# Kernel tuning notes

Hardware: AMD Instinct MI355X
Metric: run time of the kernel (lower is better)

Reference implementation:

```python
import jax, jax.numpy as jnp
import numpy as np

B, D, H, G = 32768, 768, 256, 8
GS = D // G          # group size = 96
MIN_G, MAX_G = 2, 6  # min/max active groups


def setup_inputs() -> dict:
    key = jax.random.key(0)
    ks = jax.random.split(key, 12)
    s = 0.02
    return {
        "query_embedding": jax.random.normal(ks[0], (B, D), jnp.float32),
        # router_net: Linear(D,H) -> LayerNorm(H) -> GELU -> Linear(H,H//2) -> GELU -> Linear(H//2,G)
        "w1": jax.random.normal(ks[1], (D, H), jnp.float32) * s,
        "b1": jnp.zeros((H,), jnp.float32),
        "ln_g": jnp.ones((H,), jnp.float32),
        "ln_b": jnp.zeros((H,), jnp.float32),
        "w2": jax.random.normal(ks[2], (H, H // 2), jnp.float32) * s,
        "b2": jnp.zeros((H // 2,), jnp.float32),
        "w3": jax.random.normal(ks[3], (H // 2, G), jnp.float32) * s,
        "b3": jnp.zeros((G,), jnp.float32),
        # dim_importance: Linear(D,H) -> GELU -> Linear(H,D) (bias init 2.0) -> Sigmoid
        "dw1": jax.random.normal(ks[4], (D, H), jnp.float32) * s,
        "db1": jnp.zeros((H,), jnp.float32),
        "dw2": jax.random.normal(ks[5], (H, D), jnp.float32) * s,
        "db2": jnp.full((D,), 2.0, jnp.float32),
        "group_importance": jax.random.normal(ks[6], (G,), jnp.float32) * s,
    }


def _gelu(x):
    return jax.nn.gelu(x, approximate=False)  # torch nn.GELU default = exact erf


def _layernorm(x, g, b, eps=1e-5):
    mu = jnp.mean(x, axis=-1, keepdims=True)
    var = jnp.var(x, axis=-1, keepdims=True)
    return (x - mu) * jax.lax.rsqrt(var + eps) * g + b


def reference(query_embedding, w1, b1, ln_g, ln_b, w2, b2, w3, b3,
              dw1, db1, dw2, db2, group_importance):
    x = query_embedding
    # router_net (eval mode: dropout is identity, sigmoid gating not gumbel)
    h1 = _gelu(_layernorm(x @ w1 + b1, ln_g, ln_b))
    h2 = _gelu(h1 @ w2 + b2)
    group_logits = h2 @ w3 + b3 + group_importance          # [B, G]
    group_probs = jax.nn.sigmoid(group_logits)

    # constrained hard selection: top MIN_G always on; ranks MIN_G..MAX_G-1 on iff prob > 0.5
    order = jnp.argsort(-group_probs, axis=-1)              # descending sort indices [B, G]
    sorted_probs = jnp.take_along_axis(group_probs, order, axis=-1)
    ranks = jnp.arange(G)
    act_sorted = jnp.where(ranks < MIN_G, 1.0,
                           jnp.where(ranks < MAX_G,
                                     (sorted_probs > 0.5).astype(jnp.float32), 0.0))
    b_idx = jnp.arange(x.shape[0])[:, None]
    hard_mask = jnp.zeros_like(group_probs).at[b_idx, order].set(act_sorted)
    # straight-through estimator
    group_selection = hard_mask - jax.lax.stop_gradient(group_probs) + group_probs

    # expand each group decision over its group_size dims -> [B, D]
    group_mask = jnp.repeat(group_selection, GS, axis=-1)

    dim_weights = jax.nn.sigmoid(_gelu(x @ dw1 + db1) @ dw2 + db2)  # [B, D]
    mask = group_mask * dim_weights

    active_groups = jnp.mean(jnp.sum((group_probs > 0.5).astype(jnp.float32), axis=-1))
    group_usage = jnp.mean((group_probs > 0.5).astype(jnp.float32), axis=0)
    f = jnp.mean(group_probs, axis=0)
    load_balance = G * jnp.sum(f * (1.0 / G))
    active_dims = jnp.mean(jnp.sum((mask > 0.5).astype(jnp.float32), axis=-1))

    return (mask, group_mask, dim_weights, group_probs, group_selection,
            active_groups, group_usage, load_balance, active_dims)
```

## Files before the change

kernel.cpp:

```cpp
#include <hip/hip_runtime.h>
#include <math.h>

#define NB 32768
#define ND 768
#define NH 256
#define NG 8
#define GSZ 96

typedef __attribute__((ext_vector_type(8))) short short8_t;
typedef __attribute__((ext_vector_type(4))) float f32x4;

__device__ __forceinline__ float gelu_exact(float v) {
    return 0.5f * v * (1.0f + erff(v * 0.7071067811865475f));
}
__device__ __forceinline__ float sigmoidf_(float v) {
    return 1.0f / (1.0f + expf(-v));
}
__device__ __forceinline__ unsigned short f2bf(float f) {
    union { float f; unsigned u; } a; a.f = f;
    unsigned r = a.u + 0x7FFF + ((a.u >> 16) & 1);
    return (unsigned short)(r >> 16);
}
__device__ __forceinline__ void f2bf2(float f, unsigned short& hi, unsigned short& lo) {
    union { float f; unsigned u; } a; a.f = f;
    unsigned r = a.u + 0x7FFF + ((a.u >> 16) & 1);
    hi = (unsigned short)(r >> 16);
    union { unsigned u; float f; } hf; hf.u = (r >> 16) << 16;
    float rem = f - hf.f;
    union { float f; unsigned u; } b; b.f = rem;
    unsigned r2 = b.u + 0x7FFF + ((b.u >> 16) & 1);
    lo = (unsigned short)(r2 >> 16);
}

__global__ __launch_bounds__(256) void cvt_wall(
    const float* __restrict__ w1, const float* __restrict__ dw1,
    const float* __restrict__ dw2, const float* __restrict__ w2,
    unsigned short* __restrict__ w1Th, unsigned short* __restrict__ w1Tl,
    unsigned short* __restrict__ dw1T, unsigned short* __restrict__ dw2T,
    unsigned short* __restrict__ w2Th, unsigned short* __restrict__ w2Tl,
    float* __restrict__ scal)
{
    const int b = blockIdx.x, t = threadIdx.x;
    if (b < 96) {
        int idx = b * 256 + t;
        int k8 = idx >> 8, c = idx & 255;
        short8_t h, lo;
        #pragma unroll
        for (int j = 0; j < 8; ++j) {
            unsigned short hi_, lo_;
            f2bf2(w1[(size_t)(k8 * 8 + j) * 256 + c], hi_, lo_);
            h[j] = (short)hi_; lo[j] = (short)lo_;
        }
        *(short8_t*)(w1Th + (size_t)c * 768 + k8 * 8) = h;
        *(short8_t*)(w1Tl + (size_t)c * 768 + k8 * 8) = lo;
    } else if (b < 192) {
        int idx = (b - 96) * 256 + t;
        int k8 = idx >> 8, c = idx & 255;
        short8_t h;
        #pragma unroll
        for (int j = 0; j < 8; ++j)
            h[j] = (short)f2bf(dw1[(size_t)(k8 * 8 + j) * 256 + c]);
        *(short8_t*)(dw1T + (size_t)c * 768 + k8 * 8) = h;
    } else if (b < 288) {
        int idx = (b - 192) * 256 + t;
        int k8 = idx / 768, c = idx - k8 * 768;
        short8_t h;
        #pragma unroll
        for (int j = 0; j < 8; ++j)
            h[j] = (short)f2bf(dw2[(size_t)(k8 * 8 + j) * 768 + c]);
        *(short8_t*)(dw2T + (size_t)c * 256 + k8 * 8) = h;
    } else if (b < 304) {
        int idx = (b - 288) * 256 + t;
        int k8 = idx >> 7, c = idx & 127;
        short8_t h, lo;
        #pragma unroll
        for (int j = 0; j < 8; ++j) {
            unsigned short hi_, lo_;
            f2bf2(w2[(size_t)(k8 * 8 + j) * 128 + c], hi_, lo_);
            h[j] = (short)hi_; lo[j] = (short)lo_;
        }
        *(short8_t*)(w2Th + (size_t)c * 256 + k8 * 8) = h;
        *(short8_t*)(w2Tl + (size_t)c * 256 + k8 * 8) = lo;
    } else {
        if (t < 11) scal[t] = 0.0f;
    }
}

__global__ __launch_bounds__(256) void mfma_u1(
    const float* __restrict__ x, const unsigned short* __restrict__ BTh,
    const unsigned short* __restrict__ BTl, float* __restrict__ u1)
{
    __shared__ unsigned short Ah[128][40];
    __shared__ unsigned short Al[128][40];
    __shared__ unsigned short Bh[128][40];
    __shared__ unsigned short Bl[128][40];

    const int tid = threadIdx.x;
    const int l = tid & 63;
    const int w = tid >> 6;
    const int wm = w >> 1, wn = w & 1;
    const int lg = l >> 4, lr = l & 15;
    const int rb = blockIdx.x >> 1;
    const int cb = blockIdx.x & 1;
    const int rowsBase = rb * 128, colBase = cb * 128;

    f32x4 acc[4][4];
    #pragma unroll
    for (int mi = 0; mi < 4; ++mi)
        #pragma unroll
        for (int ni = 0; ni < 4; ++ni) acc[mi][ni] = (f32x4){0.f, 0.f, 0.f, 0.f};

    for (int kb = 0; kb < ND; kb += 32) {
        #pragma unroll
        for (int m = 0; m < 2; ++m) {
            int flat = m * 256 + tid;
            int row = flat >> 2, seg = flat & 3;
            const float* src = x + (size_t)(rowsBase + row) * ND + kb + seg * 8;
            float4 v0 = *(const float4*)src;
            float4 v1 = *(const float4*)(src + 4);
            float f[8] = {v0.x, v0.y, v0.z, v0.w, v1.x, v1.y, v1.z, v1.w};
            short8_t ph, pl;
            #pragma unroll
            for (int j = 0; j < 8; ++j) {
                unsigned short hi_, lo_;
                f2bf2(f[j], hi_, lo_);
                ph[j] = (short)hi_; pl[j] = (short)lo_;
            }
            *(short8_t*)&Ah[row][seg * 8] = ph;
            *(short8_t*)&Al[row][seg * 8] = pl;
        }
        #pragma unroll
        for (int m = 0; m < 2; ++m) {
            int flat = m * 256 + tid;
            int col = flat >> 2, seg = flat & 3;
            size_t off = (size_t)(colBase + col) * ND + kb + seg * 8;
            *(short8_t*)&Bh[col][seg * 8] = *(const short8_t*)(BTh + off);
            *(short8_t*)&Bl[col][seg * 8] = *(const short8_t*)(BTl + off);
        }
        __syncthreads();

        short8_t afh[4], afl[4], bfh[4], bfl[4];
        #pragma unroll
        for (int mi = 0; mi < 4; ++mi) {
            afh[mi] = *(const short8_t*)&Ah[wm * 64 + mi * 16 + lr][lg * 8];
            afl[mi] = *(const short8_t*)&Al[wm * 64 + mi * 16 + lr][lg * 8];
        }
        #pragma unroll
        for (int ni = 0; ni < 4; ++ni) {
            bfh[ni] = *(const short8_t*)&Bh[wn * 64 + ni * 16 + lr][lg * 8];
            bfl[ni] = *(const short8_t*)&Bl[wn * 64 + ni * 16 + lr][lg * 8];
        }
        #pragma unroll
        for (int mi = 0; mi < 4; ++mi)
            #pragma unroll
            for (int ni = 0; ni < 4; ++ni) {
                acc[mi][ni] = __builtin_amdgcn_mfma_f32_16x16x32_bf16(
                    afl[mi], bfh[ni], acc[mi][ni], 0, 0, 0);
                acc[mi][ni] = __builtin_amdgcn_mfma_f32_16x16x32_bf16(
                    afh[mi], bfl[ni], acc[mi][ni], 0, 0, 0);
                acc[mi][ni] = __builtin_amdgcn_mfma_f32_16x16x32_bf16(
                    afh[mi], bfh[ni], acc[mi][ni], 0, 0, 0);
            }
        __syncthreads();
    }

    #pragma unroll
    for (int ni = 0; ni < 4; ++ni) {
        int col = colBase + wn * 64 + ni * 16 + lr;
        #pragma unroll
        for (int mi = 0; mi < 4; ++mi) {
            int rbase = rowsBase + wm * 64 + mi * 16 + lg * 4;
            #pragma unroll
            for (int j = 0; j < 4; ++j)
                u1[(size_t)(rbase + j) * 256 + col] = acc[mi][ni][j];
        }
    }
}

__global__ __launch_bounds__(256) void k1_epi(
    const float* __restrict__ u1, const float* __restrict__ b1,
    const float* __restrict__ lng, const float* __restrict__ lnb,
    float* __restrict__ h1)
{
    const int wv = threadIdx.x >> 6, l = threadIdx.x & 63;
    const int row = blockIdx.x * 4 + wv;
    float4 a = *(const float4*)(u1 + (size_t)row * 256 + l * 4);
    float4 bb = *(const float4*)(b1 + l * 4);
    float u[4] = {a.x + bb.x, a.y + bb.y, a.z + bb.z, a.w + bb.w};
    float s = u[0] + u[1] + u[2] + u[3];
    float q = u[0]*u[0] + u[1]*u[1] + u[2]*u[2] + u[3]*u[3];
    #pragma unroll
    for (int o = 1; o < 64; o <<= 1) {
        s += __shfl_xor(s, o);
        q += __shfl_xor(q, o);
    }
    float mean = s * (1.0f / 256.0f);
    float var  = q * (1.0f / 256.0f) - mean * mean;
    float rstd = rsqrtf(var + 1e-5f);
    float4 g = *(const float4*)(lng + l * 4);
    float4 be = *(const float4*)(lnb + l * 4);
    float4 o;
    o.x = gelu_exact((u[0] - mean) * rstd * g.x + be.x);
    o.y = gelu_exact((u[1] - mean) * rstd * g.y + be.y);
    o.z = gelu_exact((u[2] - mean) * rstd * g.z + be.z);
    o.w = gelu_exact((u[3] - mean) * rstd * g.w + be.w);
    *(float4*)(h1 + (size_t)row * 256 + l * 4) = o;
}

__global__ __launch_bounds__(256) void mfma_u2(
    const float* __restrict__ h1, const unsigned short* __restrict__ BTh,
    const unsigned short* __restrict__ BTl, float* __restrict__ u2)
{
    __shared__ unsigned short Ah[128][40];
    __shared__ unsigned short Al[128][40];
    __shared__ unsigned short Bh[128][40];
    __shared__ unsigned short Bl[128][40];

    const int tid = threadIdx.x;
    const int l = tid & 63;
    const int w = tid >> 6;
    const int wm = w >> 1, wn = w & 1;
    const int lg = l >> 4, lr = l & 15;
    const int rowsBase = blockIdx.x * 128;

    f32x4 acc[4][4];
    #pragma unroll
    for (int mi = 0; mi < 4; ++mi)
        #pragma unroll
        for (int ni = 0; ni < 4; ++ni) acc[mi][ni] = (f32x4){0.f, 0.f, 0.f, 0.f};

    for (int kb = 0; kb < 256; kb += 32) {
        #pragma unroll
        for (int m = 0; m < 2; ++m) {
            int flat = m * 256 + tid;
            int row = flat >> 2, seg = flat & 3;
            const float* src = h1 + (size_t)(rowsBase + row) * 256 + kb + seg * 8;
            float4 v0 = *(const float4*)src;
            float4 v1 = *(const float4*)(src + 4);
            float f[8] = {v0.x, v0.y, v0.z, v0.w, v1.x, v1.y, v1.z, v1.w};
            short8_t ph, pl;
            #pragma unroll
            for (int j = 0; j < 8; ++j) {
                unsigned short hi_, lo_;
                f2bf2(f[j], hi_, lo_);
                ph[j] = (short)hi_; pl[j] = (short)lo_;
            }
            *(short8_t*)&Ah[row][seg * 8] = ph;
            *(short8_t*)&Al[row][seg * 8] = pl;
        }
        #pragma unroll
        for (int m = 0; m < 2; ++m) {
            int flat = m * 256 + tid;
            int col = flat >> 2, seg = flat & 3;
            size_t off = (size_t)col * 256 + kb + seg * 8;
            *(short8_t*)&Bh[col][seg * 8] = *(const short8_t*)(BTh + off);
            *(short8_t*)&Bl[col][seg * 8] = *(const short8_t*)(BTl + off);
        }
        __syncthreads();

        short8_t afh[4], afl[4], bfh[4], bfl[4];
        #pragma unroll
        for (int mi = 0; mi < 4; ++mi) {
            afh[mi] = *(const short8_t*)&Ah[wm * 64 + mi * 16 + lr][lg * 8];
            afl[mi] = *(const short8_t*)&Al[wm * 64 + mi * 16 + lr][lg * 8];
        }
        #pragma unroll
        for (int ni = 0; ni < 4; ++ni) {
            bfh[ni] = *(const short8_t*)&Bh[wn * 64 + ni * 16 + lr][lg * 8];
            bfl[ni] = *(const short8_t*)&Bl[wn * 64 + ni * 16 + lr][lg * 8];
        }
        #pragma unroll
        for (int mi = 0; mi < 4; ++mi)
            #pragma unroll
            for (int ni = 0; ni < 4; ++ni) {
                acc[mi][ni] = __builtin_amdgcn_mfma_f32_16x16x32_bf16(
                    afl[mi], bfh[ni], acc[mi][ni], 0, 0, 0);
                acc[mi][ni] = __builtin_amdgcn_mfma_f32_16x16x32_bf16(
                    afh[mi], bfl[ni], acc[mi][ni], 0, 0, 0);
                acc[mi][ni] = __builtin_amdgcn_mfma_f32_16x16x32_bf16(
                    afh[mi], bfh[ni], acc[mi][ni], 0, 0, 0);
            }
        __syncthreads();
    }

    #pragma unroll
    for (int ni = 0; ni < 4; ++ni) {
        int col = wn * 64 + ni * 16 + lr;
        #pragma unroll
        for (int mi = 0; mi < 4; ++mi) {
            int rbase = rowsBase + wm * 64 + mi * 16 + lg * 4;
            #pragma unroll
            for (int j = 0; j < 4; ++j)
                u2[(size_t)(rbase + j) * 128 + col] = acc[mi][ni][j];
        }
    }
}

template<int ACT, int AF32>
__global__ __launch_bounds__(256) void mfma_hi(
    const void* __restrict__ Ap, const unsigned short* __restrict__ BT,
    const float* __restrict__ bias, void* __restrict__ outp,
    int N, int K, int colBlocks)
{
    __shared__ unsigned short As[128][40];
    __shared__ unsigned short Bs[128][40];

    const int tid = threadIdx.x;
    const int l = tid & 63;
    const int w = tid >> 6;
    const int wm = w >> 1, wn = w & 1;
    const int lg = l >> 4, lr = l & 15;
    const int rb = blockIdx.x / colBlocks;
    const int cb = blockIdx.x - rb * colBlocks;
    const int rowsBase = rb * 128, colBase = cb * 128;

    f32x4 acc[4][4];
    #pragma unroll
    for (int mi = 0; mi < 4; ++mi)
        #pragma unroll
        for (int ni = 0; ni < 4; ++ni) acc[mi][ni] = (f32x4){0.f, 0.f, 0.f, 0.f};

    for (int kb = 0; kb < K; kb += 32) {
        if (AF32) {
            const float* A = (const float*)Ap;
            #pragma unroll
            for (int m = 0; m < 2; ++m) {
                int flat = m * 256 + tid;
                int row = flat >> 2, seg = flat & 3;
                const float* src = A + (size_t)(rowsBase + row) * K + kb + seg * 8;
                float4 v0 = *(const float4*)src;
                float4 v1 = *(const float4*)(src + 4);
                float f[8] = {v0.x, v0.y, v0.z, v0.w, v1.x, v1.y, v1.z, v1.w};
                short8_t h;
                #pragma unroll
                for (int j = 0; j < 8; ++j) h[j] = (short)f2bf(f[j]);
                *(short8_t*)&As[row][seg * 8] = h;
            }
        } else {
            const unsigned short* A = (const unsigned short*)Ap;
            #pragma unroll
            for (int m = 0; m < 2; ++m) {
                int flat = m * 256 + tid;
                int row = flat >> 2, seg = flat & 3;
                *(short8_t*)&As[row][seg * 8] =
                    *(const short8_t*)(A + (size_t)(rowsBase + row) * K + kb + seg * 8);
            }
        }
        #pragma unroll
        for (int m = 0; m < 2; ++m) {
            int flat = m * 256 + tid;
            int col = flat >> 2, seg = flat & 3;
            *(short8_t*)&Bs[col][seg * 8] =
                *(const short8_t*)(BT + (size_t)(colBase + col) * K + kb + seg * 8);
        }
        __syncthreads();

        short8_t af[4], bf[4];
        #pragma unroll
        for (int mi = 0; mi < 4; ++mi)
            af[mi] = *(const short8_t*)&As[wm * 64 + mi * 16 + lr][lg * 8];
        #pragma unroll
        for (int ni = 0; ni < 4; ++ni)
            bf[ni] = *(const short8_t*)&Bs[wn * 64 + ni * 16 + lr][lg * 8];
        #pragma unroll
        for (int mi = 0; mi < 4; ++mi)
            #pragma unroll
            for (int ni = 0; ni < 4; ++ni)
                acc[mi][ni] = __builtin_amdgcn_mfma_f32_16x16x32_bf16(
                    af[mi], bf[ni], acc[mi][ni], 0, 0, 0);
        __syncthreads();
    }

    #pragma unroll
    for (int ni = 0; ni < 4; ++ni) {
        int col = colBase + wn * 64 + ni * 16 + lr;
        float bv = bias[col];
        #pragma unroll
        for (int mi = 0; mi < 4; ++mi) {
            int rbase = rowsBase + wm * 64 + mi * 16 + lg * 4;
            #pragma unroll
            for (int j = 0; j < 4; ++j) {
                float v = acc[mi][ni][j] + bv;
                if (ACT == 0) {
                    ((unsigned short*)outp)[(size_t)(rbase + j) * N + col] =
                        f2bf(gelu_exact(v));
                } else {
                    ((float*)outp)[(size_t)(rbase + j) * N + col] = sigmoidf_(v);
                }
            }
        }
    }
}

__global__ __launch_bounds__(128) void k3_router(
    const float* __restrict__ u2, const float* __restrict__ w3,
    const float* __restrict__ b3, const float* __restrict__ gi,
    const float* __restrict__ b2, float* __restrict__ probsOut,
    float* __restrict__ selOut, float* __restrict__ scal)
{
    __shared__ float ws3[128][8];
    __shared__ float sAct[2], sP[2], sCnt[2][8];

    const int tid = threadIdx.x;
    *(float4*)&ws3[tid][0] = *(const float4*)(w3 + tid * 8);
    *(float4*)&ws3[tid][4] = *(const float4*)(w3 + tid * 8 + 4);
    __syncthreads();

    const int row = blockIdx.x * 128 + tid;
    const float* r0p = u2 + (size_t)row * 128;

    float accg[8];
    #pragma unroll
    for (int g = 0; g < 8; ++g) accg[g] = 0.0f;
    #pragma unroll 4
    for (int k4 = 0; k4 < 32; ++k4) {
        float4 a = *(const float4*)(r0p + k4 * 4);
        float4 bb = *(const float4*)(b2 + k4 * 4);
        float hv4[4];
        hv4[0] = gelu_exact(a.x + bb.x);
        hv4[1] = gelu_exact(a.y + bb.y);
        hv4[2] = gelu_exact(a.z + bb.z);
        hv4[3] = gelu_exact(a.w + bb.w);
        #pragma unroll
        for (int t = 0; t < 4; ++t)
            #pragma unroll
            for (int g = 0; g < 8; ++g)
                accg[g] = fmaf(hv4[t], ws3[k4 * 4 + t][g], accg[g]);
    }

    float p[8], gs[8], cnt[8];
    float actCnt = 0.0f, pSum = 0.0f;
    #pragma unroll
    for (int g = 0; g < 8; ++g) {
        float lg = accg[g] + b3[g] + gi[g];
        p[g] = sigmoidf_(lg);
    }
    #pragma unroll
    for (int g = 0; g < 8; ++g) {
        int rank = 0;
        #pragma unroll
        for (int j = 0; j < 8; ++j) {
            rank += (p[j] > p[g]) ? 1 : 0;
            rank += (j < g && p[j] == p[g]) ? 1 : 0;
        }
        float act = (rank < 2) ? 1.0f
                  : ((rank < 6) ? ((p[g] > 0.5f) ? 1.0f : 0.0f) : 0.0f);
        gs[g] = (act - p[g]) + p[g];
        float over = (p[g] > 0.5f) ? 1.0f : 0.0f;
        cnt[g] = over;
        actCnt += over;
        pSum += p[g];
    }

    *(float4*)(probsOut + (size_t)row * 8)     = *(float4*)&p[0];
    *(float4*)(probsOut + (size_t)row * 8 + 4) = *(float4*)&p[4];
    *(float4*)(selOut   + (size_t)row * 8)     = *(float4*)&gs[0];
    *(float4*)(selOut   + (size_t)row * 8 + 4) = *(float4*)&gs[4];

    #pragma unroll
    for (int o = 32; o > 0; o >>= 1) {
        actCnt += __shfl_down(actCnt, o);
        pSum   += __shfl_down(pSum, o);
        #pragma unroll
        for (int g = 0; g < 8; ++g) cnt[g] += __shfl_down(cnt[g], o);
    }
    if ((tid & 63) == 0) {
        int w = tid >> 6;
        sAct[w] = actCnt; sP[w] = pSum;
        #pragma unroll
        for (int g = 0; g < 8; ++g) sCnt[w][g] = cnt[g];
    }
    __syncthreads();
    if (tid == 0) {
        const float invB = 1.0f / 32768.0f;
        atomicAdd(&scal[0], (sAct[0] + sAct[1]) * invB);
        atomicAdd(&scal[9], (sP[0] + sP[1]) * invB);
        #pragma unroll
        for (int g = 0; g < 8; ++g)
            atomicAdd(&scal[1 + g], (sCnt[0][g] + sCnt[1][g]) * invB);
    }
}

__global__ __launch_bounds__(512) void mfma_dw2m(
    const unsigned short* __restrict__ g1h, const unsigned short* __restrict__ dw2T,
    const float* __restrict__ db2, const float* __restrict__ sel,
    float* __restrict__ dwts, float* __restrict__ maskOut,
    float* __restrict__ activeDims)
{
    __shared__ unsigned short As[128][40];
    __shared__ unsigned short Bs[256][40];
    __shared__ float sc[8];

    const int tid = threadIdx.x;
    const int l = tid & 63;
    const int w = tid >> 6;
    const int wm = w >> 2, wn = w & 3;
    const int lg = l >> 4, lr = l & 15;
    const int rb = blockIdx.x / 3, cb = blockIdx.x - rb * 3;
    const int rowsBase = rb * 128, colBase = cb * 256;

    f32x4 acc[4][4];
    #pragma unroll
    for (int mi = 0; mi < 4; ++mi)
        #pragma unroll
        for (int ni = 0; ni < 4; ++ni) acc[mi][ni] = (f32x4){0.f, 0.f, 0.f, 0.f};

    const int sArow = tid >> 2, sAseg = tid & 3;

    for (int kb = 0; kb < 256; kb += 32) {
        *(short8_t*)&As[sArow][sAseg * 8] =
            *(const short8_t*)(g1h + (size_t)(rowsBase + sArow) * 256 + kb + sAseg * 8);
        #pragma unroll
        for (int m = 0; m < 2; ++m) {
            int flat = m * 512 + tid;
            int col = flat >> 2, seg = flat & 3;
            *(short8_t*)&Bs[col][seg * 8] =
                *(const short8_t*)(dw2T + (size_t)(colBase + col) * 256 + kb + seg * 8);
        }
        __syncthreads();

        short8_t af[4], bf[4];
        #pragma unroll
        for (int mi = 0; mi < 4; ++mi)
            af[mi] = *(const short8_t*)&As[wm * 64 + mi * 16 + lr][lg * 8];
        #pragma unroll
        for (int ni = 0; ni < 4; ++ni)
            bf[ni] = *(const short8_t*)&Bs[wn * 64 + ni * 16 + lr][lg * 8];
        #pragma unroll
        for (int mi = 0; mi < 4; ++mi)
            #pragma unroll
            for (int ni = 0; ni < 4; ++ni)
                acc[mi][ni] = __builtin_amdgcn_mfma_f32_16x16x32_bf16(
                    af[mi], bf[ni], acc[mi][ni], 0, 0, 0);
        __syncthreads();
    }

    float cntF = 0.0f;
    #pragma unroll
    for (int ni = 0; ni < 4; ++ni) {
        int col = colBase + wn * 64 + ni * 16 + lr;
        float bv = db2[col];
        int g = col / GSZ;
        #pragma unroll
        for (int mi = 0; mi < 4; ++mi) {
            int rbase = rowsBase + wm * 64 + mi * 16 + lg * 4;
            #pragma unroll
            for (int j = 0; j < 4; ++j) {
                int row = rbase + j;
                float v = sigmoidf_(acc[mi][ni][j] + bv);
                dwts[(size_t)row * 768 + col] = v;
                float m = sel[(size_t)row * 8 + g] * v;
                maskOut[(size_t)row * 768 + col] = m;
                cntF += (m > 0.5f) ? 1.0f : 0.0f;
            }
        }
    }
    #pragma unroll
    for (int o = 32; o > 0; o >>= 1) cntF += __shfl_down(cntF, o);
    if ((tid & 63) == 0) sc[tid >> 6] = cntF;
    __syncthreads();
    if (tid == 0)
        atomicAdd(activeDims, (sc[0] + sc[1] + sc[2] + sc[3] +
                               sc[4] + sc[5] + sc[6] + sc[7]) * (1.0f / 32768.0f));
}

__global__ __launch_bounds__(256) void k4_gmask(
    const float* __restrict__ sel, float* __restrict__ gmaskOut)
{
    const int stride = gridDim.x * 256;
    for (int i4 = blockIdx.x * 256 + threadIdx.x; i4 < 6291456; i4 += stride) {
        int row = i4 / 192;
        int rem = i4 - row * 192;
        int g = rem / 24;
        float v = sel[(size_t)row * 8 + g];
        float4 gm = {v, v, v, v};
        *(float4*)(gmaskOut + (size_t)i4 * 4) = gm;
    }
}

extern "C" void kernel_launch(void* const* d_in, const int* in_sizes, int n_in,
                              void* d_out, int out_size, void* d_ws, size_t ws_size,
                              hipStream_t stream)
{
    const float* x   = (const float*)d_in[0];
    const float* w1  = (const float*)d_in[1];
    const float* b1  = (const float*)d_in[2];
    const float* lng = (const float*)d_in[3];
    const float* lnb = (const float*)d_in[4];
    const float* w2  = (const float*)d_in[5];
    const float* b2  = (const float*)d_in[6];
    const float* w3  = (const float*)d_in[7];
    const float* b3  = (const float*)d_in[8];
    const float* dw1 = (const float*)d_in[9];
    const float* db1 = (const float*)d_in[10];
    const float* dw2 = (const float*)d_in[11];
    const float* db2 = (const float*)d_in[12];
    const float* gi  = (const float*)d_in[13];

    float* out   = (float*)d_out;
    float* mask  = out;
    float* gmask = out + 25165824;
    float* dwts  = out + 50331648;
    float* probs = out + 75497472;
    float* sel   = out + 75759616;
    float* scal  = out + 76021760;

    float* u1 = mask;
    float* h1 = mask + 8388608;
    float* u2 = mask + 16777216;
    unsigned short* g1h  = (unsigned short*)gmask;
    unsigned short* w1Th = (unsigned short*)(gmask + 4194304);
    unsigned short* w1Tl = (unsigned short*)(gmask + 4292608);
    unsigned short* dw1T = (unsigned short*)(gmask + 4390912);
    unsigned short* dw2T = (unsigned short*)(gmask + 4489216);
    unsigned short* w2Th = (unsigned short*)(gmask + 4587520);
    unsigned short* w2Tl = (unsigned short*)(gmask + 4603904);

    cvt_wall<<<dim3(305), dim3(256), 0, stream>>>(
        w1, dw1, dw2, w2, w1Th, w1Tl, dw1T, dw2T, w2Th, w2Tl, scal);
    mfma_u1<<<dim3(512), dim3(256), 0, stream>>>(x, w1Th, w1Tl, u1);
    mfma_hi<0, 1><<<dim3(512), dim3(256), 0, stream>>>(
        (const void*)x, dw1T, db1, (void*)g1h, 256, 768, 2);
    k1_epi<<<dim3(8192), dim3(256), 0, stream>>>(u1, b1, lng, lnb, h1);
    mfma_u2<<<dim3(256), dim3(256), 0, stream>>>(h1, w2Th, w2Tl, u2);
    k3_router<<<dim3(256), dim3(128), 0, stream>>>(
        u2, w3, b3, gi, b2, probs, sel, scal);
    mfma_dw2m<<<dim3(768), dim3(512), 0, stream>>>(
        g1h, dw2T, db2, sel, dwts, mask, &scal[10]);
    k4_gmask<<<dim3(2048), dim3(256), 0, stream>>>(sel, gmask);
}
```

Before: 276.0 us.

## Fuse group-mask write into dw2 GEMM epilogue and widen u1 tile

mfma_u1 now runs 512-thread blocks that cover all 256 output columns per 128-row tile, so each x row is loaded and split into bf16 hi/lo only once instead of twice. When a large enough workspace buffer is available, the bf16 intermediates move there, which frees the group-mask output region. The dw2 epilogue then writes group_mask directly, so the separate k4_gmask pass and its re-read of sel are skipped. Without a workspace the old separate kernel path is kept. The wider block doubles B-tile shared memory and may lower occupancy.

```diff
diff --git a/kernel.cpp b/kernel.cpp
--- a/kernel.cpp
+++ b/kernel.cpp
@@ -86,23 +86,21 @@
     }
 }
 
-__global__ __launch_bounds__(256) void mfma_u1(
+__global__ __launch_bounds__(512) void mfma_u1(
     const float* __restrict__ x, const unsigned short* __restrict__ BTh,
     const unsigned short* __restrict__ BTl, float* __restrict__ u1)
 {
     __shared__ unsigned short Ah[128][40];
     __shared__ unsigned short Al[128][40];
-    __shared__ unsigned short Bh[128][40];
-    __shared__ unsigned short Bl[128][40];
+    __shared__ unsigned short Bh[256][40];
+    __shared__ unsigned short Bl[256][40];
 
     const int tid = threadIdx.x;
     const int l = tid & 63;
     const int w = tid >> 6;
-    const int wm = w >> 1, wn = w & 1;
+    const int wm = w >> 2, wn = w & 3;
     const int lg = l >> 4, lr = l & 15;
-    const int rb = blockIdx.x >> 1;
-    const int cb = blockIdx.x & 1;
-    const int rowsBase = rb * 128, colBase = cb * 128;
+    const int rowsBase = blockIdx.x * 128;
 
     f32x4 acc[4][4];
     #pragma unroll
@@ -110,12 +108,11 @@
         #pragma unroll
         for (int ni = 0; ni < 4; ++ni) acc[mi][ni] = (f32x4){0.f, 0.f, 0.f, 0.f};
 
+    const int sArow = tid >> 2, sAseg = tid & 3;
+
     for (int kb = 0; kb < ND; kb += 32) {
-        #pragma unroll
-        for (int m = 0; m < 2; ++m) {
-            int flat = m * 256 + tid;
-            int row = flat >> 2, seg = flat & 3;
-            const float* src = x + (size_t)(rowsBase + row) * ND + kb + seg * 8;
+        {
+            const float* src = x + (size_t)(rowsBase + sArow) * ND + kb + sAseg * 8;
             float4 v0 = *(const float4*)src;
             float4 v1 = *(const float4*)(src + 4);
             float f[8] = {v0.x, v0.y, v0.z, v0.w, v1.x, v1.y, v1.z, v1.w};
@@ -126,14 +123,14 @@
                 f2bf2(f[j], hi_, lo_);
                 ph[j] = (short)hi_; pl[j] = (short)lo_;
             }
-            *(short8_t*)&Ah[row][seg * 8] = ph;
-            *(short8_t*)&Al[row][seg * 8] = pl;
+            *(short8_t*)&Ah[sArow][sAseg * 8] = ph;
+            *(short8_t*)&Al[sArow][sAseg * 8] = pl;
         }
         #pragma unroll
         for (int m = 0; m < 2; ++m) {
-            int flat = m * 256 + tid;
+            int flat = m * 512 + tid;
             int col = flat >> 2, seg = flat & 3;
-            size_t off = (size_t)(colBase + col) * ND + kb + seg * 8;
+            size_t off = (size_t)col * ND + kb + seg * 8;
             *(short8_t*)&Bh[col][seg * 8] = *(const short8_t*)(BTh + off);
             *(short8_t*)&Bl[col][seg * 8] = *(const short8_t*)(BTl + off);
         }
@@ -166,7 +163,7 @@
 
     #pragma unroll
     for (int ni = 0; ni < 4; ++ni) {
-        int col = colBase + wn * 64 + ni * 16 + lr;
+        int col = wn * 64 + ni * 16 + lr;
         #pragma unroll
         for (int mi = 0; mi < 4; ++mi) {
             int rbase = rowsBase + wm * 64 + mi * 16 + lg * 4;
@@ -485,7 +482,7 @@
     const unsigned short* __restrict__ g1h, const unsigned short* __restrict__ dw2T,
     const float* __restrict__ db2, const float* __restrict__ sel,
     float* __restrict__ dwts, float* __restrict__ maskOut,
-    float* __restrict__ activeDims)
+    float* __restrict__ gmaskOut, float* __restrict__ activeDims)
 {
     __shared__ unsigned short As[128][40];
     __shared__ unsigned short Bs[256][40];
@@ -547,10 +544,12 @@
             #pragma unroll
             for (int j = 0; j < 4; ++j) {
                 int row = rbase + j;
+                float sv = sel[(size_t)row * 8 + g];
                 float v = sigmoidf_(acc[mi][ni][j] + bv);
                 dwts[(size_t)row * 768 + col] = v;
-                float m = sel[(size_t)row * 8 + g] * v;
+                float m = sv * v;
                 maskOut[(size_t)row * 768 + col] = m;
+                if (gmaskOut) gmaskOut[(size_t)row * 768 + col] = sv;
                 cntF += (m > 0.5f) ? 1.0f : 0.0f;
             }
         }
@@ -608,17 +607,35 @@
     float* u1 = mask;
     float* h1 = mask + 8388608;
     float* u2 = mask + 16777216;
-    unsigned short* g1h  = (unsigned short*)gmask;
-    unsigned short* w1Th = (unsigned short*)(gmask + 4194304);
-    unsigned short* w1Tl = (unsigned short*)(gmask + 4292608);
-    unsigned short* dw1T = (unsigned short*)(gmask + 4390912);
-    unsigned short* dw2T = (unsigned short*)(gmask + 4489216);
-    unsigned short* w2Th = (unsigned short*)(gmask + 4587520);
-    unsigned short* w2Tl = (unsigned short*)(gmask + 4603904);
+
+    const size_t WS_NEED = 16777216ULL
+                         + 393216ULL * 4
+                         + 65536ULL * 2;
+    bool useWs = (d_ws != nullptr) && (ws_size >= WS_NEED);
+
+    unsigned short *g1h, *w1Th, *w1Tl, *dw1T, *dw2T, *w2Th, *w2Tl;
+    if (useWs) {
+        char* wsb = (char*)d_ws;
+        g1h  = (unsigned short*)(wsb);
+        w1Th = (unsigned short*)(wsb + 16777216);
+        w1Tl = (unsigned short*)(wsb + 16777216 + 393216);
+        dw1T = (unsigned short*)(wsb + 16777216 + 393216 * 2);
+        dw2T = (unsigned short*)(wsb + 16777216 + 393216 * 3);
+        w2Th = (unsigned short*)(wsb + 16777216 + 393216 * 4);
+        w2Tl = (unsigned short*)(wsb + 16777216 + 393216 * 4 + 65536);
+    } else {
+        g1h  = (unsigned short*)gmask;
+        w1Th = (unsigned short*)(gmask + 4194304);
+        w1Tl = (unsigned short*)(gmask + 4292608);
+        dw1T = (unsigned short*)(gmask + 4390912);
+        dw2T = (unsigned short*)(gmask + 4489216);
+        w2Th = (unsigned short*)(gmask + 4587520);
+        w2Tl = (unsigned short*)(gmask + 4603904);
+    }
 
     cvt_wall<<<dim3(305), dim3(256), 0, stream>>>(
         w1, dw1, dw2, w2, w1Th, w1Tl, dw1T, dw2T, w2Th, w2Tl, scal);
-    mfma_u1<<<dim3(512), dim3(256), 0, stream>>>(x, w1Th, w1Tl, u1);
+    mfma_u1<<<dim3(256), dim3(512), 0, stream>>>(x, w1Th, w1Tl, u1);
     mfma_hi<0, 1><<<dim3(512), dim3(256), 0, stream>>>(
         (const void*)x, dw1T, db1, (void*)g1h, 256, 768, 2);
     k1_epi<<<dim3(8192), dim3(256), 0, stream>>>(u1, b1, lng, lnb, h1);
@@ -626,6 +643,7 @@
     k3_router<<<dim3(256), dim3(128), 0, stream>>>(
         u2, w3, b3, gi, b2, probs, sel, scal);
     mfma_dw2m<<<dim3(768), dim3(512), 0, stream>>>(
-        g1h, dw2T, db2, sel, dwts, mask, &scal[10]);
-    k4_gmask<<<dim3(2048), dim3(256), 0, stream>>>(sel, gmask);
-}
+        g1h, dw2T, db2, sel, dwts, mask, useWs ? gmask : nullptr, &scal[10]);
+    if (!useWs)
+        k4_gmask<<<dim3(2048), dim3(256), 0, stream>>>(sel, gmask);
+}
```

After: 286.1 us. +3.7%, slower.
